# Optimization experiments

Measured on AMD Instinct MI355X. Metric: run time of the kernel, lower is better.

The kernel has to match this reference:

```python
import jax, jax.numpy as jnp
import numpy as np

B, S, HID = 1, 2048, 2048   # batch, block_size, hidden_dim
H, D = 16, 128              # num_heads, head_dim
WORLD_SIZE = 4
LOCAL_BLOCK_IDX = 3         # last rank: all kv blocks are causally visible


def setup_inputs() -> dict:
    key = jax.random.key(0)
    ks = jax.random.split(key, 5)
    w = lambda k: jax.random.normal(k, (H * D, HID), dtype=jnp.float32) * 0.02
    return {
        "hidden_states": jax.random.normal(ks[0], (B, S, HID), dtype=jnp.float32),
        "q_w": w(ks[1]), "q_b": jnp.zeros((H * D,), jnp.float32),
        "k_w": w(ks[2]), "k_b": jnp.zeros((H * D,), jnp.float32),
        "v_w": w(ks[3]), "v_b": jnp.zeros((H * D,), jnp.float32),
        "o_w": jax.random.normal(ks[4], (HID, H * D), dtype=jnp.float32) * 0.02,
        "o_b": jnp.zeros((HID,), jnp.float32),
        "world_size": WORLD_SIZE,
        "local_block_idx": LOCAL_BLOCK_IDX,
    }


def reference(hidden_states, q_w, q_b, k_w, k_b, v_w, v_b, o_w, o_b,
              world_size, local_block_idx):
    Bsz, Sq, _ = hidden_states.shape

    def proj(w, b):  # (B,S,HID) -> (B,H,S,D)
        return (hidden_states @ w.T + b).reshape(Bsz, Sq, H, D).transpose(0, 2, 1, 3)

    q, k, v = proj(q_w, q_b), proj(k_w, k_b), proj(v_w, v_b)
    scale = D ** -0.5

    # ring_send_recv is a local copy, so K/V are identical every ring step;
    # only the causal masking differs (triu mask on the diagonal block step).
    scores_base = jnp.einsum('bhqd,bhkd->bhqk', q, k) * scale
    tri = jnp.triu(jnp.ones((Sq, Sq), bool), k=1)
    scores_diag = jnp.where(tri, -jnp.inf, scores_base)

    out = jnp.zeros((Bsz, H, Sq, D), hidden_states.dtype)
    mx = jnp.full((Bsz, H, Sq, 1), -jnp.inf, hidden_states.dtype)
    se = jnp.zeros((Bsz, H, Sq, 1), hidden_states.dtype)

    for step in range(world_size):  # small fixed ring loop
        kv_idx = (local_block_idx - step) % world_size
        scores = scores_diag if kv_idx == local_block_idx else scores_base
        # OnlineSoftmax.update (faithful, including block-wise normalization)
        bm = scores.max(axis=-1, keepdims=True)
        nm = jnp.maximum(mx, bm)
        old_s = jnp.exp(mx - nm)
        new_s = jnp.exp(bm - nm)
        be = jnp.exp(scores - bm)
        bs = be.sum(axis=-1, keepdims=True)
        se = se * old_s + bs * new_s
        aw = be / (bs + 1e-8)
        bo = jnp.einsum('bhqk,bhkd->bhqd', aw, v)
        out = out * old_s + bo * new_s
        mx = nm

    out = out / (se + 1e-8)  # OnlineSoftmax.finalize
    out = out.transpose(0, 2, 1, 3).reshape(Bsz, Sq, H * D)
    return out @ o_w.T + o_b
```

## Files before the change

kernel.cpp:

```cpp
#include <hip/hip_runtime.h>
#include <hip/hip_bf16.h>
#include <stdint.h>
#include <stddef.h>


typedef __attribute__((ext_vector_type(8))) short bf16x8;
typedef __attribute__((ext_vector_type(4))) float f32x4;

#define MFMA_BF16(a, b, c) __builtin_amdgcn_mfma_f32_16x16x32_bf16((a), (b), (c), 0, 0, 0)

__device__ __forceinline__ void load16_lds(const void* g, void* l) {
  __builtin_amdgcn_global_load_lds((const __attribute__((address_space(1))) void*)g,
                                   (__attribute__((address_space(3))) void*)l,
                                   16, 0, 0);
}

__device__ __forceinline__ unsigned short f2bf(float x) {
  union { __hip_bfloat16 b; unsigned short u; } cv;
  cv.b = __float2bfloat16(x);
  return cv.u;
}

__global__ __launch_bounds__(256) void cvt_all(
    const float4* __restrict__ s0, const float4* __restrict__ s1,
    const float4* __restrict__ s2, const float4* __restrict__ s3,
    const float4* __restrict__ s4,
    ushort4* __restrict__ d0, ushort4* __restrict__ d1,
    ushort4* __restrict__ d2, ushort4* __restrict__ d3,
    ushort4* __restrict__ d4) {
  const int seg = blockIdx.x >> 12;
  const int i = ((blockIdx.x & 4095) << 8) + threadIdx.x;
  const float4* s = seg == 0 ? s0 : seg == 1 ? s1 : seg == 2 ? s2 : seg == 3 ? s3 : s4;
  ushort4* d = seg == 0 ? d0 : seg == 1 ? d1 : seg == 2 ? d2 : seg == 3 ? d3 : d4;
  float4 v = s[i];
  ushort4 o;
  o.x = f2bf(v.x); o.y = f2bf(v.y); o.z = f2bf(v.z); o.w = f2bf(v.w);
  d[i] = o;
}

__global__ __launch_bounds__(256) void gemm_qkv(
    const unsigned short* __restrict__ A, const unsigned short* __restrict__ Bt,
    const float* __restrict__ qb, const float* __restrict__ kb,
    const float* __restrict__ vb,
    unsigned short* __restrict__ Qo, unsigned short* __restrict__ Ko,
    unsigned short* __restrict__ Vt) {
  __shared__ __align__(16) unsigned short sA[128 * 64];
  __shared__ __align__(16) unsigned short sB[128 * 64];
  const int tid = threadIdx.x;
  const int wave = tid >> 6, lane = tid & 63;
  const int quad = lane >> 4, l16 = lane & 15;
  const int wr = wave >> 1, wc = wave & 1;
  const int m0 = blockIdx.y << 7, n0 = blockIdx.x << 7;

  f32x4 acc[4][4] = {};

  for (int k0 = 0; k0 < 2048; k0 += 64) {
    __syncthreads();
#pragma unroll
    for (int t = 0; t < 4; t++) {
      const int i = t * 4 + wave;
      const int idx = i * 64 + lane;
      const int row = idx >> 3;
      const int c = (idx & 7) ^ (row & 7);
      load16_lds(A + (size_t)(m0 + row) * 2048 + k0 + c * 8, &sA[i * 512]);
      load16_lds(Bt + (size_t)(n0 + row) * 2048 + k0 + c * 8, &sB[i * 512]);
    }
    __syncthreads();
#pragma unroll
    for (int ks = 0; ks < 2; ks++) {
      bf16x8 af[4], bfr[4];
#pragma unroll
      for (int i = 0; i < 4; i++) {
        const int cs = ((ks * 4 + quad) ^ (l16 & 7)) << 3;
        af[i] = *(const bf16x8*)&sA[(wr * 64 + i * 16 + l16) * 64 + cs];
        bfr[i] = *(const bf16x8*)&sB[(wc * 64 + i * 16 + l16) * 64 + cs];
      }
#pragma unroll
      for (int mi = 0; mi < 4; mi++)
#pragma unroll
        for (int ni = 0; ni < 4; ni++)
          acc[mi][ni] = MFMA_BF16(af[mi], bfr[ni], acc[mi][ni]);
    }
  }

  const float qscale = 0.088388347648318447f * 1.4426950408889634f;
#pragma unroll
  for (int mi = 0; mi < 4; mi++) {
    const int row = m0 + wr * 64 + mi * 16 + quad * 4;
#pragma unroll
    for (int ni = 0; ni < 4; ni++) {
      const int col = n0 + wc * 64 + ni * 16 + l16;
#pragma unroll
      for (int r = 0; r < 4; r++) {
        const float v = acc[mi][ni][r];
        const int rr = row + r;
        if (col < 2048) {
          const int hh = col >> 7, d = col & 127;
          Qo[((size_t)hh * 2048 + rr) * 128 + d] = f2bf((v + qb[col]) * qscale);
        } else if (col < 4096) {
          const int f = col - 2048;
          const int hh = f >> 7, d = f & 127;
          Ko[((size_t)hh * 2048 + rr) * 128 + d] = f2bf(v + kb[f]);
        } else {
          const int f = col - 4096;
          const int hh = f >> 7, d = f & 127;
          Vt[((size_t)hh * 128 + d) * 2048 + rr] = f2bf(v + vb[f]);
        }
      }
    }
  }
}

__global__ __launch_bounds__(128, 1) void attn_fwd(
    const unsigned short* __restrict__ Q, const unsigned short* __restrict__ K,
    const unsigned short* __restrict__ V,
    unsigned short* __restrict__ O,
    const int* __restrict__ wsp) {
  const int qt = blockIdx.x, h = blockIdx.y;
  const int tid = threadIdx.x;
  const int wave = tid >> 6, lane = tid & 63;
  const int quad = lane >> 4, l16 = lane & 15;

  __shared__ __align__(16) unsigned short sK0[64 * 128];
  __shared__ __align__(16) unsigned short sK1[64 * 128];
  __shared__ __align__(16) unsigned short sV0[128 * 64];
  __shared__ __align__(16) unsigned short sV1[128 * 64];
  __shared__ __align__(16) unsigned short sP[2 * 2 * 1024];

  const unsigned short* Qh = Q + (size_t)h * 2048 * 128;
  const unsigned short* Kh = K + (size_t)h * 2048 * 128;
  const unsigned short* Vh = V + (size_t)h * 128 * 2048;

  for (int c = wave; c < 16; c += 2) {
    const int rowc = lane >> 4;
    const int row = c * 4 + rowc;
    const int blk = (lane & 15) ^ (row & 15);
    load16_lds(Qh + (size_t)(qt * 64 + row) * 128 + blk * 8, &sK0[c * 512]);
  }
  __syncthreads();

  bf16x8 qf[2][4];
#pragma unroll
  for (int s = 0; s < 2; s++)
#pragma unroll
    for (int ds = 0; ds < 4; ds++)
      qf[s][ds] = *(const bf16x8*)&sK0[(wave * 32 + s * 16 + l16) * 128 +
                                       (((ds * 4 + quad) ^ l16) << 3)];
  __syncthreads();

  float m1[2] = {-3.0e38f, -3.0e38f}, l1[2] = {0.f, 0.f};
  float m2[2] = {-3.0e38f, -3.0e38f}, l2[2] = {0.f, 0.f};
  f32x4 o1[2][8], o2[2][8];
#pragma unroll
  for (int s = 0; s < 2; s++)
#pragma unroll
    for (int j = 0; j < 8; j++) {
      o1[s][j] = f32x4{0.f, 0.f, 0.f, 0.f};
      o2[s][j] = f32x4{0.f, 0.f, 0.f, 0.f};
    }

  auto stageKV = [&](int kt, unsigned short* kDst, unsigned short* vDst) {
    const int k0 = kt << 6;
    for (int c = wave; c < 16; c += 2) {
      {
        const int rowc = lane >> 4;
        const int row = c * 4 + rowc;
        const int blk = (lane & 15) ^ (row & 15);
        load16_lds(Kh + (size_t)(k0 + row) * 128 + blk * 8, &kDst[c * 512]);
      }
      {
        const int rowc = lane >> 3;
        const int row = c * 8 + rowc;
        const int blk = (lane & 7) ^ (rowc & 7);
        load16_lds(Vh + (size_t)row * 2048 + k0 + blk * 8, &vDst[c * 512]);
      }
    }
  };

  auto softmax_update = [&](int sub, float& m, float& l, f32x4 (&o)[8],
                            const f32x4 (&stt)[4], bool masked, int k0) {
    const int qg = qt * 64 + wave * 32 + sub * 16 + l16;
    float t[4][4];
    float mx = -3.0e38f;
#pragma unroll
    for (int ni = 0; ni < 4; ni++)
#pragma unroll
      for (int r = 0; r < 4; r++) {
        float v = stt[ni][r];
        if (masked && (k0 + ni * 16 + quad * 4 + r > qg)) v = -3.0e38f;
        t[ni][r] = v;
        mx = fmaxf(mx, v);
      }
    mx = fmaxf(mx, __shfl_xor(mx, 16));
    mx = fmaxf(mx, __shfl_xor(mx, 32));
    const float mn = fmaxf(m, mx);
    const float al = exp2f(m - mn);
    unsigned short* sPw = &sP[(wave * 2 + sub) * 1024];
    float rs = 0.f;
#pragma unroll
    for (int ni = 0; ni < 4; ni++) {
      union { unsigned short u[4]; uint2 v; } pk;
#pragma unroll
      for (int r = 0; r < 4; r++) {
        const float p = exp2f(t[ni][r] - mn);
        rs += p;
        pk.u[r] = f2bf(p);
      }
      const int off =
          l16 * 64 + (((ni * 2 + (quad >> 1)) ^ (l16 & 7)) << 3) + ((quad & 1) << 2);
      *(uint2*)&sPw[off] = pk.v;
    }
    rs += __shfl_xor(rs, 16);
    rs += __shfl_xor(rs, 32);
    const bool grew = !__all(mn == m);
    l = l * al + rs;
    m = mn;
    if (grew) {
#pragma unroll
      for (int r = 0; r < 4; r++) {
        const int src = (lane & 48) + quad * 4 + r;
        const float ab = __shfl(al, src);
#pragma unroll
        for (int j = 0; j < 8; j++) o[j][r] *= ab;
      }
    }
  };

  auto pv_shared = [&](f32x4 (&oo)[2][8], const unsigned short* vBuf) {
#pragma unroll
    for (int ks = 0; ks < 2; ks++) {
      const int cs = (((ks * 4 + quad) ^ (l16 & 7)) << 3);
      const bf16x8 pf0 = *(const bf16x8*)&sP[(wave * 2 + 0) * 1024 + l16 * 64 + cs];
      const bf16x8 pf1 = *(const bf16x8*)&sP[(wave * 2 + 1) * 1024 + l16 * 64 + cs];
#pragma unroll
      for (int j = 0; j < 8; j++) {
        const bf16x8 vf = *(const bf16x8*)&vBuf[(j * 16 + l16) * 64 + cs];
        oo[0][j] = MFMA_BF16(pf0, vf, oo[0][j]);
        oo[1][j] = MFMA_BF16(pf1, vf, oo[1][j]);
      }
    }
  };

  auto compute_tile = [&](int kt, const unsigned short* kBuf,
                          const unsigned short* vBuf) {
    const int k0 = kt << 6;
    f32x4 st[2][4];
#pragma unroll
    for (int s = 0; s < 2; s++)
#pragma unroll
      for (int ni = 0; ni < 4; ni++) st[s][ni] = f32x4{0.f, 0.f, 0.f, 0.f};
#pragma unroll
    for (int ds = 0; ds < 4; ds++) {
#pragma unroll
      for (int ni = 0; ni < 4; ni++) {
        const bf16x8 kf =
            *(const bf16x8*)&kBuf[(ni * 16 + l16) * 128 + (((ds * 4 + quad) ^ l16) << 3)];
        st[0][ni] = MFMA_BF16(kf, qf[0][ds], st[0][ni]);
        st[1][ni] = MFMA_BF16(kf, qf[1][ds], st[1][ni]);
      }
    }

    if (kt == qt) {
#pragma unroll
      for (int s = 0; s < 2; s++) {
        m1[s] = m2[s]; l1[s] = l2[s];
#pragma unroll
        for (int j = 0; j < 8; j++) o1[s][j] = o2[s][j];
      }
      softmax_update(0, m1[0], l1[0], o1[0], st[0], true, k0);
      softmax_update(1, m1[1], l1[1], o1[1], st[1], true, k0);
      pv_shared(o1, vBuf);
    }
    softmax_update(0, m2[0], l2[0], o2[0], st[0], false, k0);
    softmax_update(1, m2[1], l2[1], o2[1], st[1], false, k0);
    pv_shared(o2, vBuf);
  };

  stageKV(0, sK0, sV0);
  for (int kt2 = 0; kt2 < 32; kt2 += 2) {
    __syncthreads();
    if (kt2 + 1 < 32) stageKV(kt2 + 1, sK1, sV1);
    compute_tile(kt2, sK0, sV0);
    __syncthreads();
    if (kt2 + 2 < 32) stageKV(kt2 + 2, sK0, sV0);
    compute_tile(kt2 + 1, sK1, sV1);
  }

  const float fws = (float)(wsp[0] - 1);
#pragma unroll
  for (int s = 0; s < 2; s++) {
    const float a = exp2f(m1[s] - m2[s]);
    const float se = l1[s] * a + fws * l2[s];
    const float inv = 1.0f / (se + 1e-8f);
    const float f1 = (a / (l1[s] + 1e-8f)) * inv;
    const float f2 = (fws / (l2[s] + 1e-8f)) * inv;
#pragma unroll
    for (int r = 0; r < 4; r++) {
      const int src = (lane & 48) + quad * 4 + r;
      const float f1b = __shfl(f1, src);
      const float f2b = __shfl(f2, src);
      const int row = qt * 64 + wave * 32 + s * 16 + quad * 4 + r;
#pragma unroll
      for (int j = 0; j < 8; j++) {
        const float ov = o1[s][j][r] * f1b + o2[s][j][r] * f2b;
        O[(size_t)row * 2048 + h * 128 + j * 16 + l16] = f2bf(ov);
      }
    }
  }
}

__global__ __launch_bounds__(256) void gemm_o(
    const unsigned short* __restrict__ A, const unsigned short* __restrict__ Bt,
    const float* __restrict__ ob, float* __restrict__ Cout) {
  __shared__ __align__(16) unsigned short sA[64 * 128];
  __shared__ __align__(16) unsigned short sB[128 * 128];
  const int tid = threadIdx.x;
  const int wave = tid >> 6, lane = tid & 63;
  const int quad = lane >> 4, l16 = lane & 15;
  const int wm = wave >> 1, wn = wave & 1;
  const int m0 = blockIdx.y << 6, n0 = blockIdx.x << 7;

  f32x4 acc[2][4] = {};

  for (int k0 = 0; k0 < 2048; k0 += 128) {
    __syncthreads();
#pragma unroll
    for (int t = 0; t < 4; t++) {
      const int i = t * 4 + wave;
      const int idx = i * 64 + lane;
      const int row = idx >> 4;
      const int c = (idx & 15) ^ (row & 15);
      load16_lds(A + (size_t)(m0 + row) * 2048 + k0 + c * 8, &sA[i * 512]);
    }
#pragma unroll
    for (int t = 0; t < 8; t++) {
      const int i = t * 4 + wave;
      const int idx = i * 64 + lane;
      const int row = idx >> 4;
      const int c = (idx & 15) ^ (row & 15);
      load16_lds(Bt + (size_t)(n0 + row) * 2048 + k0 + c * 8, &sB[i * 512]);
    }
    __syncthreads();
#pragma unroll
    for (int ks = 0; ks < 4; ks++) {
      const int cs = ((ks * 4 + quad) ^ l16) << 3;
      bf16x8 af[2], bfr[4];
#pragma unroll
      for (int i = 0; i < 2; i++)
        af[i] = *(const bf16x8*)&sA[(wm * 32 + i * 16 + l16) * 128 + cs];
#pragma unroll
      for (int i = 0; i < 4; i++)
        bfr[i] = *(const bf16x8*)&sB[(wn * 64 + i * 16 + l16) * 128 + cs];
#pragma unroll
      for (int mi = 0; mi < 2; mi++)
#pragma unroll
        for (int ni = 0; ni < 4; ni++)
          acc[mi][ni] = MFMA_BF16(af[mi], bfr[ni], acc[mi][ni]);
    }
  }

#pragma unroll
  for (int mi = 0; mi < 2; mi++) {
    const int row = m0 + wm * 32 + mi * 16 + quad * 4;
#pragma unroll
    for (int ni = 0; ni < 4; ni++) {
      const int col = n0 + wn * 64 + ni * 16 + l16;
#pragma unroll
      for (int r = 0; r < 4; r++) {
        Cout[(size_t)(row + r) * 2048 + col] = acc[mi][ni][r] + ob[col];
      }
    }
  }
}

extern "C" void kernel_launch(void* const* d_in, const int* in_sizes, int n_in,
                              void* d_out, int out_size, void* d_ws, size_t ws_size,
                              hipStream_t stream) {
  (void)in_sizes; (void)n_in; (void)out_size; (void)ws_size;
  const float* hs = (const float*)d_in[0];
  const float* qw = (const float*)d_in[1];
  const float* qb = (const float*)d_in[2];
  const float* kw = (const float*)d_in[3];
  const float* kb = (const float*)d_in[4];
  const float* vw = (const float*)d_in[5];
  const float* vb = (const float*)d_in[6];
  const float* ow = (const float*)d_in[7];
  const float* ob = (const float*)d_in[8];
  const int* wsz = (const int*)d_in[9];

  char* w = (char*)d_ws;
  unsigned short* hsb  = (unsigned short*)(w + 0);
  unsigned short* wqkv = (unsigned short*)(w + 8388608);
  unsigned short* owb  = (unsigned short*)(w + 33554432);
  unsigned short* Qb_  = (unsigned short*)(w + 41943040);
  unsigned short* Kb_  = (unsigned short*)(w + 50331648);
  unsigned short* Vtb  = (unsigned short*)(w + 58720256);
  unsigned short* atb  = (unsigned short*)(w + 67108864);

  cvt_all<<<20480, 256, 0, stream>>>(
      (const float4*)hs, (const float4*)qw, (const float4*)kw, (const float4*)vw,
      (const float4*)ow,
      (ushort4*)hsb, (ushort4*)wqkv, (ushort4*)(wqkv + 4194304),
      (ushort4*)(wqkv + 8388608), (ushort4*)owb);

  gemm_qkv<<<dim3(48, 16), 256, 0, stream>>>(hsb, wqkv, qb, kb, vb, Qb_, Kb_, Vtb);
  attn_fwd<<<dim3(32, 16), 128, 0, stream>>>(Qb_, Kb_, Vtb, atb, wsz);
  gemm_o<<<dim3(16, 32), 256, 0, stream>>>(atb, owb, ob, (float*)d_out);
}
```

Baseline: 347.2 us.

## Split attention block across four waves with sixteen query rows each

The attention kernel now runs 256 threads (4 waves) per 64-row query tile instead of 2 waves, so each wave owns 16 query rows rather than 32. This halves the per-wave accumulator and Q-fragment register state and lets two blocks share a CU. The intent is more parallel waves to hide latency and raise occupancy. In exchange, each K/V fragment read from LDS is reused across fewer MFMAs, so LDS read traffic per FLOP doubles.

```diff
diff --git a/kernel.cpp b/kernel.cpp
--- a/kernel.cpp
+++ b/kernel.cpp
@@ -111,7 +111,7 @@
   }
 }
 
-__global__ __launch_bounds__(128, 1) void attn_fwd(
+__global__ __launch_bounds__(256, 2) void attn_fwd(
     const unsigned short* __restrict__ Q, const unsigned short* __restrict__ K,
     const unsigned short* __restrict__ V,
     unsigned short* __restrict__ O,
@@ -125,13 +125,14 @@
   __shared__ __align__(16) unsigned short sK1[64 * 128];
   __shared__ __align__(16) unsigned short sV0[128 * 64];
   __shared__ __align__(16) unsigned short sV1[128 * 64];
-  __shared__ __align__(16) unsigned short sP[2 * 2 * 1024];
+  __shared__ __align__(16) unsigned short sP[4][16 * 64];
 
   const unsigned short* Qh = Q + (size_t)h * 2048 * 128;
   const unsigned short* Kh = K + (size_t)h * 2048 * 128;
   const unsigned short* Vh = V + (size_t)h * 128 * 2048;
-
-  for (int c = wave; c < 16; c += 2) {
+  unsigned short* sPw = sP[wave];
+
+  for (int c = wave; c < 16; c += 4) {
     const int rowc = lane >> 4;
     const int row = c * 4 + rowc;
     const int blk = (lane & 15) ^ (row & 15);
@@ -139,29 +140,20 @@
   }
   __syncthreads();
 
-  bf16x8 qf[2][4];
-#pragma unroll
-  for (int s = 0; s < 2; s++)
-#pragma unroll
-    for (int ds = 0; ds < 4; ds++)
-      qf[s][ds] = *(const bf16x8*)&sK0[(wave * 32 + s * 16 + l16) * 128 +
-                                       (((ds * 4 + quad) ^ l16) << 3)];
+  bf16x8 qf[4];
+#pragma unroll
+  for (int ds = 0; ds < 4; ds++)
+    qf[ds] = *(const bf16x8*)&sK0[(wave * 16 + l16) * 128 + (((ds * 4 + quad) ^ l16) << 3)];
   __syncthreads();
 
-  float m1[2] = {-3.0e38f, -3.0e38f}, l1[2] = {0.f, 0.f};
-  float m2[2] = {-3.0e38f, -3.0e38f}, l2[2] = {0.f, 0.f};
-  f32x4 o1[2][8], o2[2][8];
-#pragma unroll
-  for (int s = 0; s < 2; s++)
-#pragma unroll
-    for (int j = 0; j < 8; j++) {
-      o1[s][j] = f32x4{0.f, 0.f, 0.f, 0.f};
-      o2[s][j] = f32x4{0.f, 0.f, 0.f, 0.f};
-    }
+  float m1 = -3.0e38f, l1 = 0.f, m2 = -3.0e38f, l2 = 0.f;
+  f32x4 o1[8], o2[8];
+#pragma unroll
+  for (int j = 0; j < 8; j++) { o1[j] = f32x4{0.f, 0.f, 0.f, 0.f}; o2[j] = f32x4{0.f, 0.f, 0.f, 0.f}; }
 
   auto stageKV = [&](int kt, unsigned short* kDst, unsigned short* vDst) {
     const int k0 = kt << 6;
-    for (int c = wave; c < 16; c += 2) {
+    for (int c = wave; c < 16; c += 4) {
       {
         const int rowc = lane >> 4;
         const int row = c * 4 + rowc;
@@ -177,9 +169,9 @@
     }
   };
 
-  auto softmax_update = [&](int sub, float& m, float& l, f32x4 (&o)[8],
+  auto softmax_update = [&](float& m, float& l, f32x4 (&o)[8],
                             const f32x4 (&stt)[4], bool masked, int k0) {
-    const int qg = qt * 64 + wave * 32 + sub * 16 + l16;
+    const int qg = qt * 64 + wave * 16 + l16;
     float t[4][4];
     float mx = -3.0e38f;
 #pragma unroll
@@ -195,7 +187,6 @@
     mx = fmaxf(mx, __shfl_xor(mx, 32));
     const float mn = fmaxf(m, mx);
     const float al = exp2f(m - mn);
-    unsigned short* sPw = &sP[(wave * 2 + sub) * 1024];
     float rs = 0.f;
 #pragma unroll
     for (int ni = 0; ni < 4; ni++) {
@@ -226,17 +217,15 @@
     }
   };
 
-  auto pv_shared = [&](f32x4 (&oo)[2][8], const unsigned short* vBuf) {
+  auto pv = [&](f32x4 (&o)[8], const unsigned short* vBuf) {
 #pragma unroll
     for (int ks = 0; ks < 2; ks++) {
       const int cs = (((ks * 4 + quad) ^ (l16 & 7)) << 3);
-      const bf16x8 pf0 = *(const bf16x8*)&sP[(wave * 2 + 0) * 1024 + l16 * 64 + cs];
-      const bf16x8 pf1 = *(const bf16x8*)&sP[(wave * 2 + 1) * 1024 + l16 * 64 + cs];
+      const bf16x8 pf = *(const bf16x8*)&sPw[l16 * 64 + cs];
 #pragma unroll
       for (int j = 0; j < 8; j++) {
         const bf16x8 vf = *(const bf16x8*)&vBuf[(j * 16 + l16) * 64 + cs];
-        oo[0][j] = MFMA_BF16(pf0, vf, oo[0][j]);
-        oo[1][j] = MFMA_BF16(pf1, vf, oo[1][j]);
+        o[j] = MFMA_BF16(pf, vf, o[j]);
       }
     }
   };
@@ -244,36 +233,28 @@
   auto compute_tile = [&](int kt, const unsigned short* kBuf,
                           const unsigned short* vBuf) {
     const int k0 = kt << 6;
-    f32x4 st[2][4];
-#pragma unroll
-    for (int s = 0; s < 2; s++)
-#pragma unroll
-      for (int ni = 0; ni < 4; ni++) st[s][ni] = f32x4{0.f, 0.f, 0.f, 0.f};
+    f32x4 st[4];
+#pragma unroll
+    for (int ni = 0; ni < 4; ni++) st[ni] = f32x4{0.f, 0.f, 0.f, 0.f};
 #pragma unroll
     for (int ds = 0; ds < 4; ds++) {
 #pragma unroll
       for (int ni = 0; ni < 4; ni++) {
         const bf16x8 kf =
             *(const bf16x8*)&kBuf[(ni * 16 + l16) * 128 + (((ds * 4 + quad) ^ l16) << 3)];
-        st[0][ni] = MFMA_BF16(kf, qf[0][ds], st[0][ni]);
-        st[1][ni] = MFMA_BF16(kf, qf[1][ds], st[1][ni]);
+        st[ni] = MFMA_BF16(kf, qf[ds], st[ni]);
       }
     }
 
     if (kt == qt) {
-#pragma unroll
-      for (int s = 0; s < 2; s++) {
-        m1[s] = m2[s]; l1[s] = l2[s];
-#pragma unroll
-        for (int j = 0; j < 8; j++) o1[s][j] = o2[s][j];
-      }
-      softmax_update(0, m1[0], l1[0], o1[0], st[0], true, k0);
-      softmax_update(1, m1[1], l1[1], o1[1], st[1], true, k0);
-      pv_shared(o1, vBuf);
-    }
-    softmax_update(0, m2[0], l2[0], o2[0], st[0], false, k0);
-    softmax_update(1, m2[1], l2[1], o2[1], st[1], false, k0);
-    pv_shared(o2, vBuf);
+      m1 = m2; l1 = l2;
+#pragma unroll
+      for (int j = 0; j < 8; j++) o1[j] = o2[j];
+      softmax_update(m1, l1, o1, st, true, k0);
+      pv(o1, vBuf);
+    }
+    softmax_update(m2, l2, o2, st, false, k0);
+    pv(o2, vBuf);
   };
 
   stageKV(0, sK0, sV0);
@@ -287,24 +268,21 @@
   }
 
   const float fws = (float)(wsp[0] - 1);
-#pragma unroll
-  for (int s = 0; s < 2; s++) {
-    const float a = exp2f(m1[s] - m2[s]);
-    const float se = l1[s] * a + fws * l2[s];
-    const float inv = 1.0f / (se + 1e-8f);
-    const float f1 = (a / (l1[s] + 1e-8f)) * inv;
-    const float f2 = (fws / (l2[s] + 1e-8f)) * inv;
-#pragma unroll
-    for (int r = 0; r < 4; r++) {
-      const int src = (lane & 48) + quad * 4 + r;
-      const float f1b = __shfl(f1, src);
-      const float f2b = __shfl(f2, src);
-      const int row = qt * 64 + wave * 32 + s * 16 + quad * 4 + r;
-#pragma unroll
-      for (int j = 0; j < 8; j++) {
-        const float ov = o1[s][j][r] * f1b + o2[s][j][r] * f2b;
-        O[(size_t)row * 2048 + h * 128 + j * 16 + l16] = f2bf(ov);
-      }
+  const float a = exp2f(m1 - m2);
+  const float se = l1 * a + fws * l2;
+  const float inv = 1.0f / (se + 1e-8f);
+  const float f1 = (a / (l1 + 1e-8f)) * inv;
+  const float f2 = (fws / (l2 + 1e-8f)) * inv;
+#pragma unroll
+  for (int r = 0; r < 4; r++) {
+    const int src = (lane & 48) + quad * 4 + r;
+    const float f1b = __shfl(f1, src);
+    const float f2b = __shfl(f2, src);
+    const int row = qt * 64 + wave * 16 + quad * 4 + r;
+#pragma unroll
+    for (int j = 0; j < 8; j++) {
+      const float ov = o1[j][r] * f1b + o2[j][r] * f2b;
+      O[(size_t)row * 2048 + h * 128 + j * 16 + l16] = f2bf(ov);
     }
   }
 }
@@ -404,6 +382,6 @@
       (ushort4*)(wqkv + 8388608), (ushort4*)owb);
 
   gemm_qkv<<<dim3(48, 16), 256, 0, stream>>>(hsb, wqkv, qb, kb, vb, Qb_, Kb_, Vtb);
-  attn_fwd<<<dim3(32, 16), 128, 0, stream>>>(Qb_, Kb_, Vtb, atb, wsz);
+  attn_fwd<<<dim3(32, 16), 256, 0, stream>>>(Qb_, Kb_, Vtb, atb, wsz);
   gemm_o<<<dim3(16, 32), 256, 0, stream>>>(atb, owb, ob, (float*)d_out);
 }
```

After: 322.4 us. 7.2% less time.
